# Optimization experiments

Hardware: AMD Instinct MI355X
Metric: run time of the kernel (lower is better)

Reference implementation:

```python
import jax, jax.numpy as jnp
import numpy as np

N, IN_DIM, HID = 8192, 128, 256
LEAKY_SLOPE = 0.01  # torch nn.LeakyReLU default


def setup_inputs() -> dict:
    key = jax.random.key(0)
    k1, k2, k3, k4, k5 = jax.random.split(key, 5)
    X = jax.random.normal(k1, (N, IN_DIM), jnp.float32)
    E = jax.random.uniform(k2, (N, N), jnp.float32)  # positive so DS row sums are safe
    W = jax.random.normal(k3, (HID, IN_DIM), jnp.float32) / np.sqrt(IN_DIM)
    b = jnp.zeros((HID,), jnp.float32)
    Ai = jax.random.normal(k4, (1, IN_DIM), jnp.float32)
    Aj = jax.random.normal(k5, (1, IN_DIM), jnp.float32)
    return {"X": X, "E": E, "W": W, "b": b, "Ai": Ai, "Aj": Aj}


def _ds(Ep):
    # Faithful to the original: rows of Ep are row-sum-normalized then
    # torch.cat'ed into a FLAT 1-D vector e of length N*hidden_dim; S is the
    # total sum; ehat[i, j] = e[i] * e[j] / S for i, j < N (an outer product
    # of the first N flat entries). This replaces the O(N^2) python loop.
    n = Ep.shape[0]
    flat = (Ep / jnp.sum(Ep, axis=1, keepdims=True)).reshape(-1)  # [N*HID]
    S = jnp.sum(flat)
    v = flat[:n]  # first N flattened entries
    return jnp.outer(v, v) / S  # [N, N]


def reference(X, E, W, b, Ai, Aj):
    Xh = X @ W.T + b  # [N, HID]
    a = Xh * (jnp.sum(Ai) + jnp.sum(Aj))  # Ai.sum(1)/Aj.sum(1) are scalars
    Ep = E @ jnp.exp(jax.nn.leaky_relu(a, LEAKY_SLOPE))  # [N, HID]
    alpha = _ds(Ep)  # [N, N]
    out = jax.nn.softmax((alpha @ X) @ W.T + b, axis=1)  # [N, HID]
    return (out, alpha)
```

## Files before the change

kernel.cpp:

```cpp
#include <hip/hip_runtime.h>


#define LEAKY 0.01f
constexpr float INV_S = 1.0f / 8192.0f;

typedef float v4f __attribute__((ext_vector_type(4)));

__global__ __launch_bounds__(256) void k_g(const float* __restrict__ X,
                                           const float* __restrict__ W,
                                           const float* __restrict__ b,
                                           const float* __restrict__ Ai,
                                           const float* __restrict__ Aj,
                                           float* __restrict__ g) {
    __shared__ float4 Xs[16 * 32];
    __shared__ float sred[4];
    int tid = threadIdx.x;

    float val = (tid < 128) ? Ai[tid] : Aj[tid - 128];
    for (int off = 32; off > 0; off >>= 1) val += __shfl_down(val, off, 64);
    if ((tid & 63) == 0) sred[tid >> 6] = val;

    int row0 = blockIdx.x * 16;
    const float4* X4 = (const float4*)(X + (size_t)row0 * 128);
    Xs[tid] = X4[tid];
    Xs[tid + 256] = X4[tid + 256];
    __syncthreads();

    float s = sred[0] + sred[1] + sred[2] + sred[3];
    float bk = b[tid];
    const float4* W4 = (const float4*)(W + (size_t)tid * 128);

    float acc[16];
#pragma unroll
    for (int r = 0; r < 16; r++) acc[r] = 0.f;

    for (int c4 = 0; c4 < 32; c4++) {
        float4 w = W4[c4];
#pragma unroll
        for (int r = 0; r < 16; r++) {
            float4 x = Xs[r * 32 + c4];
            acc[r] += w.x * x.x + w.y * x.y + w.z * x.z + w.w * x.w;
        }
    }
#pragma unroll
    for (int r = 0; r < 16; r++) {
        float a = s * (acc[r] + bk);
        float lr = (a >= 0.f) ? a : LEAKY * a;
        g[(size_t)(row0 + r) * 256 + tid] = expf(lr);
    }
}

__global__ __launch_bounds__(256) void k_ep(const float* __restrict__ E,
                                            const float* __restrict__ g,
                                            float* __restrict__ part) {
    __shared__ float4 Es4[32][16];
    int tid = threadIdx.x;
    int p = blockIdx.x;
    int m0 = p * 64;
    {
        int j = tid >> 3;
        int q = tid & 7;
        const float4* Erow = (const float4*)(E + (size_t)j * 8192 + m0);
        Es4[j][q] = Erow[q];
        Es4[j][q + 8] = Erow[q + 8];
    }
    __syncthreads();

    float acc[32];
#pragma unroll
    for (int j = 0; j < 32; j++) acc[j] = 0.f;

    const float* gp = g + (size_t)m0 * 256 + tid;
#pragma unroll 2
    for (int mg = 0; mg < 16; mg++) {
        float gv0 = gp[(size_t)(mg * 4 + 0) * 256];
        float gv1 = gp[(size_t)(mg * 4 + 1) * 256];
        float gv2 = gp[(size_t)(mg * 4 + 2) * 256];
        float gv3 = gp[(size_t)(mg * 4 + 3) * 256];
#pragma unroll
        for (int j = 0; j < 32; j++) {
            float4 e = Es4[j][mg];
            acc[j] += e.x * gv0 + e.y * gv1 + e.z * gv2 + e.w * gv3;
        }
    }
#pragma unroll
    for (int j = 0; j < 32; j++)
        part[((size_t)j * 128 + p) * 256 + tid] = acc[j];
}

__global__ __launch_bounds__(1024) void k_v(const float* __restrict__ part,
                                            float* __restrict__ v) {
    int tid = threadIdx.x;
    int k = tid & 255;
    int q = tid >> 8;
    int j = blockIdx.x;
    const float* base = part + (size_t)j * 128 * 256 + k;
    float a = 0.f;
    for (int p = q * 32; p < q * 32 + 32; p++) a += base[(size_t)p * 256];
    __shared__ float red[1024];
    red[tid] = a;
    __syncthreads();
    float ep = 0.f;
    if (q == 0) ep = red[k] + red[k + 256] + red[k + 512] + red[k + 768];
    float w = ep;
    for (int off = 32; off > 0; off >>= 1) w += __shfl_down(w, off, 64);
    __shared__ float red4[16];
    if ((tid & 63) == 0) red4[tid >> 6] = w;
    __syncthreads();
    if (q == 0) {
        float r = red4[0] + red4[1] + red4[2] + red4[3];
        v[(size_t)j * 256 + k] = ep / r;
    }
}

__global__ __launch_bounds__(256) void k_u(const float* __restrict__ X,
                                           const float* __restrict__ v,
                                           float* __restrict__ upart) {
    int tid = threadIdx.x;
    int c = tid & 127;
    int h = tid >> 7;
    int i0 = blockIdx.x * 32 + h * 16;
    float acc = 0.f;
    for (int t = 0; t < 16; t++) {
        int i = i0 + t;
        acc += v[i] * X[(size_t)i * 128 + c];
    }
    __shared__ float red[256];
    red[tid] = acc;
    __syncthreads();
    if (tid < 128) upart[(size_t)blockIdx.x * 128 + tid] = red[tid] + red[tid + 128];
}

__global__ __launch_bounds__(256) void k_y(const float* __restrict__ upart,
                                           const float* __restrict__ W,
                                           float* __restrict__ y) {
    __shared__ float u[128];
    int k = threadIdx.x;
    if (k < 128) {
        float a = 0.f;
        for (int bb = 0; bb < 256; bb++) a += upart[(size_t)bb * 128 + k];
        u[k] = a;
    }
    __syncthreads();
    float acc = 0.f;
    for (int c = 0; c < 128; c++) acc += W[(size_t)k * 128 + c] * u[c];
    y[k] = acc;
}

__global__ __launch_bounds__(256) void k_out_alpha(const float* __restrict__ v,
                                                   const float* __restrict__ y,
                                                   const float* __restrict__ b,
                                                   float* __restrict__ out,
                                                   float* __restrict__ alpha) {
    int k = threadIdx.x;
    float yk = y[k];
    float bk = b[k];
    const float4* v4 = (const float4*)v;
    float4 vv[8];
#pragma unroll
    for (int jj = 0; jj < 8; jj++) vv[jj] = v4[k + jj * 256];
    __shared__ float red[4];
#pragma unroll 1
    for (int rr = 0; rr < 4; rr++) {
        int i = blockIdx.x * 4 + rr;
        float vi = v[i] * INV_S;
        float z = vi * yk + bk;
        float m = z;
        for (int off = 32; off > 0; off >>= 1) m = fmaxf(m, __shfl_down(m, off, 64));
        if ((k & 63) == 0) red[k >> 6] = m;
        __syncthreads();
        m = fmaxf(fmaxf(red[0], red[1]), fmaxf(red[2], red[3]));
        __syncthreads();
        float e = expf(z - m);
        float ssum = e;
        for (int off = 32; off > 0; off >>= 1) ssum += __shfl_down(ssum, off, 64);
        if ((k & 63) == 0) red[k >> 6] = ssum;
        __syncthreads();
        ssum = red[0] + red[1] + red[2] + red[3];
        out[(size_t)i * 256 + k] = e / ssum;

        float* A = alpha + (size_t)i * 8192;
#pragma unroll
        for (int jj = 0; jj < 8; jj++) {
            float4 t = vv[jj];
            v4f sv = {t.x * vi, t.y * vi, t.z * vi, t.w * vi};
            __builtin_nontemporal_store(sv, (v4f*)A + k + jj * 256);
        }
        __syncthreads();
    }
}

extern "C" void kernel_launch(void* const* d_in, const int* in_sizes, int n_in,
                              void* d_out, int out_size, void* d_ws, size_t ws_size,
                              hipStream_t stream) {
    const float* X  = (const float*)d_in[0];
    const float* E  = (const float*)d_in[1];
    const float* W  = (const float*)d_in[2];
    const float* b  = (const float*)d_in[3];
    const float* Ai = (const float*)d_in[4];
    const float* Aj = (const float*)d_in[5];

    float* out   = (float*)d_out;
    float* alpha = out + 2097152;

    float* part  = alpha;

    float* ws    = (float*)d_ws;
    float* g     = ws;
    float* v     = g + 2097152;
    float* upart = v + 8192;
    float* y     = upart + 32768;

    k_g<<<512, 256, 0, stream>>>(X, W, b, Ai, Aj, g);
    k_ep<<<128, 256, 0, stream>>>(E, g, part);
    k_v<<<32, 1024, 0, stream>>>(part, v);
    k_u<<<256, 256, 0, stream>>>(X, v, upart);
    k_y<<<1, 256, 0, stream>>>(upart, W, y);
    k_out_alpha<<<2048, 256, 0, stream>>>(v, y, b, out, alpha);
}
```

Baseline: 517.4 us.

## Fuse v/u/y kernels into neighbors and batch softmax reductions in output kernel

Merges the u-partial reduction into the v-normalization kernel and moves the tiny W·u matvec into every block of the output kernel. This removes two launches, including a single-block serial kernel. The output kernel now batches the four rows' max and sum reductions so they share barriers. It also replaces the nontemporal alpha stores with plain float4 stores. In exchange, each of the 2048 blocks redundantly sums the upart partials and recomputes the 256x128 matvec, and the plain stores may pollute cache on the 256MB alpha write.

Result: faster. 458.3 us (-11.4%).

```diff
diff --git a/kernel.cpp b/kernel.cpp
--- a/kernel.cpp
+++ b/kernel.cpp
@@ -3,8 +3,6 @@
 
 #define LEAKY 0.01f
 constexpr float INV_S = 1.0f / 8192.0f;
-
-typedef float v4f __attribute__((ext_vector_type(4)));
 
 __global__ __launch_bounds__(256) void k_g(const float* __restrict__ X,
                                            const float* __restrict__ W,
@@ -88,105 +86,125 @@
         part[((size_t)j * 128 + p) * 256 + tid] = acc[j];
 }
 
-__global__ __launch_bounds__(1024) void k_v(const float* __restrict__ part,
-                                            float* __restrict__ v) {
+__global__ __launch_bounds__(1024) void k_vu(const float* __restrict__ part,
+                                             const float* __restrict__ X,
+                                             float* __restrict__ v,
+                                             float* __restrict__ upart) {
     int tid = threadIdx.x;
     int k = tid & 255;
     int q = tid >> 8;
     int j = blockIdx.x;
+
     const float* base = part + (size_t)j * 128 * 256 + k;
     float a = 0.f;
     for (int p = q * 32; p < q * 32 + 32; p++) a += base[(size_t)p * 256];
     __shared__ float red[1024];
+    __shared__ float v_s[256];
+    __shared__ float red4[16];
     red[tid] = a;
     __syncthreads();
+
     float ep = 0.f;
     if (q == 0) ep = red[k] + red[k + 256] + red[k + 512] + red[k + 768];
     float w = ep;
     for (int off = 32; off > 0; off >>= 1) w += __shfl_down(w, off, 64);
-    __shared__ float red4[16];
     if ((tid & 63) == 0) red4[tid >> 6] = w;
     __syncthreads();
     if (q == 0) {
         float r = red4[0] + red4[1] + red4[2] + red4[3];
-        v[(size_t)j * 256 + k] = ep / r;
-    }
-}
-
-__global__ __launch_bounds__(256) void k_u(const float* __restrict__ X,
-                                           const float* __restrict__ v,
-                                           float* __restrict__ upart) {
-    int tid = threadIdx.x;
+        float vk = ep / r;
+        v[(size_t)j * 256 + k] = vk;
+        v_s[k] = vk;
+    }
+    __syncthreads();
+
     int c = tid & 127;
-    int h = tid >> 7;
-    int i0 = blockIdx.x * 32 + h * 16;
+    int grp = tid >> 7;
+    const float* Xp = X + ((size_t)j * 256 + grp * 32) * 128 + c;
     float acc = 0.f;
-    for (int t = 0; t < 16; t++) {
-        int i = i0 + t;
-        acc += v[i] * X[(size_t)i * 128 + c];
-    }
-    __shared__ float red[256];
+#pragma unroll 4
+    for (int t = 0; t < 32; t++) acc += v_s[grp * 32 + t] * Xp[(size_t)t * 128];
     red[tid] = acc;
     __syncthreads();
-    if (tid < 128) upart[(size_t)blockIdx.x * 128 + tid] = red[tid] + red[tid + 128];
-}
-
-__global__ __launch_bounds__(256) void k_y(const float* __restrict__ upart,
-                                           const float* __restrict__ W,
-                                           float* __restrict__ y) {
-    __shared__ float u[128];
-    int k = threadIdx.x;
-    if (k < 128) {
-        float a = 0.f;
-        for (int bb = 0; bb < 256; bb++) a += upart[(size_t)bb * 128 + k];
-        u[k] = a;
-    }
-    __syncthreads();
-    float acc = 0.f;
-    for (int c = 0; c < 128; c++) acc += W[(size_t)k * 128 + c] * u[c];
-    y[k] = acc;
+    if (tid < 128) {
+        float s = 0.f;
+#pragma unroll
+        for (int gg = 0; gg < 8; gg++) s += red[gg * 128 + tid];
+        upart[(size_t)j * 128 + tid] = s;
+    }
 }
 
 __global__ __launch_bounds__(256) void k_out_alpha(const float* __restrict__ v,
-                                                   const float* __restrict__ y,
+                                                   const float* __restrict__ upart,
+                                                   const float* __restrict__ W,
                                                    const float* __restrict__ b,
                                                    float* __restrict__ out,
                                                    float* __restrict__ alpha) {
+    __shared__ float u_s[128];
+    __shared__ float redm[4][4];
+    __shared__ float reds[4][4];
     int k = threadIdx.x;
-    float yk = y[k];
-    float bk = b[k];
+
+    if (k < 128) {
+        float s = 0.f;
+#pragma unroll 8
+        for (int jb = 0; jb < 32; jb++) s += upart[(size_t)jb * 128 + k];
+        u_s[k] = s;
+    }
     const float4* v4 = (const float4*)v;
     float4 vv[8];
 #pragma unroll
     for (int jj = 0; jj < 8; jj++) vv[jj] = v4[k + jj * 256];
-    __shared__ float red[4];
-#pragma unroll 1
-    for (int rr = 0; rr < 4; rr++) {
-        int i = blockIdx.x * 4 + rr;
-        float vi = v[i] * INV_S;
-        float z = vi * yk + bk;
-        float m = z;
-        for (int off = 32; off > 0; off >>= 1) m = fmaxf(m, __shfl_down(m, off, 64));
-        if ((k & 63) == 0) red[k >> 6] = m;
-        __syncthreads();
-        m = fmaxf(fmaxf(red[0], red[1]), fmaxf(red[2], red[3]));
-        __syncthreads();
-        float e = expf(z - m);
-        float ssum = e;
-        for (int off = 32; off > 0; off >>= 1) ssum += __shfl_down(ssum, off, 64);
-        if ((k & 63) == 0) red[k >> 6] = ssum;
-        __syncthreads();
-        ssum = red[0] + red[1] + red[2] + red[3];
-        out[(size_t)i * 256 + k] = e / ssum;
-
-        float* A = alpha + (size_t)i * 8192;
+    __syncthreads();
+
+    const float4* W4 = (const float4*)(W + (size_t)k * 128);
+    const float4* u4 = (const float4*)u_s;
+    float yk = 0.f;
+#pragma unroll 8
+    for (int c4 = 0; c4 < 32; c4++) {
+        float4 w = W4[c4];
+        float4 uu = u4[c4];
+        yk += w.x * uu.x + w.y * uu.y + w.z * uu.z + w.w * uu.w;
+    }
+    float bk = b[k];
+    int i0 = blockIdx.x * 4;
+
+    float vi[4], e[4];
+#pragma unroll
+    for (int rr = 0; rr < 4; rr++) {
+        vi[rr] = v[i0 + rr] * INV_S;
+        float z = vi[rr] * yk + bk;
+        float mm = z;
+        for (int off = 32; off > 0; off >>= 1) mm = fmaxf(mm, __shfl_down(mm, off, 64));
+        if ((k & 63) == 0) redm[rr][k >> 6] = mm;
+        e[rr] = z;
+    }
+    __syncthreads();
+#pragma unroll
+    for (int rr = 0; rr < 4; rr++) {
+        float mm = fmaxf(fmaxf(redm[rr][0], redm[rr][1]), fmaxf(redm[rr][2], redm[rr][3]));
+        float ee = expf(e[rr] - mm);
+        e[rr] = ee;
+        float ss = ee;
+        for (int off = 32; off > 0; off >>= 1) ss += __shfl_down(ss, off, 64);
+        if ((k & 63) == 0) reds[rr][k >> 6] = ss;
+    }
+    __syncthreads();
+#pragma unroll
+    for (int rr = 0; rr < 4; rr++) {
+        float ss = reds[rr][0] + reds[rr][1] + reds[rr][2] + reds[rr][3];
+        out[(size_t)(i0 + rr) * 256 + k] = e[rr] / ss;
+    }
+
+#pragma unroll
+    for (int rr = 0; rr < 4; rr++) {
+        float sc = vi[rr];
+        float4* A4 = (float4*)(alpha + (size_t)(i0 + rr) * 8192);
 #pragma unroll
         for (int jj = 0; jj < 8; jj++) {
             float4 t = vv[jj];
-            v4f sv = {t.x * vi, t.y * vi, t.z * vi, t.w * vi};
-            __builtin_nontemporal_store(sv, (v4f*)A + k + jj * 256);
+            A4[k + jj * 256] = make_float4(t.x * sc, t.y * sc, t.z * sc, t.w * sc);
         }
-        __syncthreads();
     }
 }
 
@@ -209,12 +227,9 @@
     float* g     = ws;
     float* v     = g + 2097152;
     float* upart = v + 8192;
-    float* y     = upart + 32768;
 
     k_g<<<512, 256, 0, stream>>>(X, W, b, Ai, Aj, g);
     k_ep<<<128, 256, 0, stream>>>(E, g, part);
-    k_v<<<32, 1024, 0, stream>>>(part, v);
-    k_u<<<256, 256, 0, stream>>>(X, v, upart);
-    k_y<<<1, 256, 0, stream>>>(upart, W, y);
-    k_out_alpha<<<2048, 256, 0, stream>>>(v, y, b, out, alpha);
-}
+    k_vu<<<32, 1024, 0, stream>>>(part, X, v, upart);
+    k_out_alpha<<<2048, 256, 0, stream>>>(v, upart, W, b, out, alpha);
+}
```
